# Performance work log

Measured on AMD Instinct MI355X. Metric: run time of the kernel, lower is better.

## Reference

```python
import jax, jax.numpy as jnp
import numpy as np

N, F, T, C = 20000, 4, 12, 256
HID, OUT = 128, 12
ER, E = 30000, 320000


def _gcn_agg(xw, src, dst, w):
    """GCNConv propagation with self-loops (weight 1): D^-1/2 (A+I) D^-1/2 @ xw.
    xw: [N, T, C] pre-projected features; src/dst: [E] int; w: [E] edge weights."""
    n = xw.shape[0]
    deg = jnp.zeros((n,), xw.dtype).at[dst].add(w) + 1.0  # +1 from self-loop
    dinv = jax.lax.rsqrt(deg)
    coef = (dinv[src] * w * dinv[dst])[:, None, None]      # [E,1,1]
    out = jnp.zeros_like(xw).at[dst].add(coef * xw[src])   # scatter-add messages
    return out + (dinv * dinv)[:, None, None] * xw         # self-loop term


def _regional_conv(x, Wc, bc, regs):
    # Shared GCNConv applied to each of the 5 state graphs, outputs summed.
    xw = jnp.einsum("nft,fc->ntc", x, Wc)  # [N, T, C], all periods at once
    out = bc
    for (src, dst, w) in regs:
        out = out + _gcn_agg(xw, src, dst, w)
    return out


def _forward(x, attrs, idxs, Wc_z, bc_z, Wl_z, bl_z, Wc_h, bc_h, Wl_h, bl_h,
             attention, W1, b1, W2, b2):
    regs = [(idx[0], idx[1], w) for idx, w in zip(idxs, attrs)]
    # A3TGCN runs an independent TGCN-GRU step per period from H=None (zeros),
    # then attention-averages over periods. With H=0:
    #   Z = sigmoid(linear_z([conv_z(X_t), 0]))   (hidden half of Wl drops out)
    #   reset gate R multiplies H=0, so it has no effect on the output
    #   H_tilde = tanh(linear_h([conv_h(X_t), 0]));  H_t = (1-Z)*H_tilde
    cz = _regional_conv(x, Wc_z, bc_z, regs)         # [N, T, C]
    Z = jax.nn.sigmoid(cz @ Wl_z[:C] + bl_z)
    ch = _regional_conv(x, Wc_h, bc_h, regs)
    Htilde = jnp.tanh(ch @ Wl_h[:C] + bl_h)
    Ht = (1.0 - Z) * Htilde                          # [N, T, C]
    probs = jax.nn.softmax(attention)                # [T]
    h = jnp.einsum("ntc,t->nc", Ht, probs)           # temporal attention pooling
    y = jax.nn.relu(h)
    y = jax.nn.relu(y @ W1 + b1)
    y = y @ W2 + b2
    return y, h


def setup_inputs():
    key = jax.random.key(0)
    ks = jax.random.split(key, 32)
    s = 0.05
    inp = {
        "x": jax.random.normal(ks[0], (N, F, T), jnp.float32),
        "edge_index": jax.random.randint(ks[1], (2, E), 0, N, jnp.int32),
    }
    regions = ["IA", "KS", "KY", "OH", "WI"]
    for i, nm in enumerate(regions):
        inp[nm + "edge_index"] = jax.random.randint(ks[2 + i], (2, ER), 0, N, jnp.int32)
    for i, nm in enumerate(regions):
        inp[nm + "edge_attr"] = jax.random.uniform(ks[7 + i], (ER,), jnp.float32)
    for gi, g in enumerate(["z", "r", "h"]):
        inp["Wc_" + g] = jax.random.normal(ks[12 + gi], (F, C), jnp.float32) * s
        inp["bc_" + g] = jnp.zeros((C,), jnp.float32)
        inp["Wl_" + g] = jax.random.normal(ks[15 + gi], (2 * C, C), jnp.float32) * s
        inp["bl_" + g] = jnp.zeros((C,), jnp.float32)
    inp["attention"] = jax.random.normal(ks[18], (T,), jnp.float32)
    inp["W1"] = jax.random.normal(ks[19], (C, HID), jnp.float32) * s
    inp["b1"] = jnp.zeros((HID,), jnp.float32)
    inp["W2"] = jax.random.normal(ks[20], (HID, OUT), jnp.float32) * s
    inp["b2"] = jnp.zeros((OUT,), jnp.float32)
    return inp


def reference(x, edge_index, IAedge_index, KSedge_index, KYedge_index, OHedge_index, WIedge_index,
              IAedge_attr, KSedge_attr, KYedge_attr, OHedge_attr, WIedge_attr,
              Wc_z, bc_z, Wl_z, bl_z, Wc_r, bc_r, Wl_r, bl_r, Wc_h, bc_h, Wl_h, bl_h,
              attention, W1, b1, W2, b2):
    # The full-graph edge_index and the reset-gate parameters are carried by the
    # original module but cannot influence the output (regional convs use the 5
    # state graphs; the reset gate multiplies the zero initial hidden state).
    idxs = [IAedge_index, KSedge_index, KYedge_index, OHedge_index, WIedge_index]
    attrs = [IAedge_attr, KSedge_attr, KYedge_attr, OHedge_attr, WIedge_attr]
    return _forward(x, attrs, idxs, Wc_z, bc_z, Wl_z, bl_z, Wc_h, bc_h, Wl_h, bl_h,
                    attention, W1, b1, W2, b2)
```

## Files before the change

### kernel.cpp

```cpp
#include <hip/hip_runtime.h>

constexpr int N    = 20000;
constexpr int T    = 12;
constexpr int C    = 256;
constexpr int HIDN = 128;
constexpr int OUTD = 12;
constexpr int ER   = 30000;
constexpr int NFT  = 48;
constexpr int EDGE_TOT = 5 * ER;
constexpr int CAP      = 32;
constexpr int EB       = 586;
constexpr int NT       = N / 16;

constexpr int WS_DEG    = 0;
constexpr int WS_CNT    = 100000;
constexpr int WS_MV     = 120000;
constexpr int WS_ZEND   = 122576;
constexpr int WS_WP     = 122576;
constexpr int WS_W2T    = 138960;
constexpr int WS_BUCKET = 140496;

constexpr float LOG2E = 1.4426950408889634f;

typedef __attribute__((ext_vector_type(8))) short short8;
typedef __attribute__((ext_vector_type(4))) float floatx4;
typedef __attribute__((ext_vector_type(2))) float floatx2;

#if __has_builtin(__builtin_amdgcn_exp2f)
#define EXP2(x) __builtin_amdgcn_exp2f(x)
#else
#define EXP2(x) exp2f(x)
#endif

__device__ __forceinline__ floatx2 pk_fma(floatx2 a, floatx2 b, floatx2 c) {
  floatx2 r;
  r.x = fmaf(a.x, b.x, c.x);
  r.y = fmaf(a.y, b.y, c.y);
  return r;
}

__device__ __forceinline__ short f2bf(float f) {
  unsigned u = __float_as_uint(f);
  u = u + 0x7fffu + ((u >> 16) & 1u);
  return (short)(u >> 16);
}

__device__ __forceinline__ void pick_region(
    int r,
    const int* e0, const int* e1, const int* e2, const int* e3, const int* e4,
    const float* a0, const float* a1, const float* a2, const float* a3, const float* a4,
    const int*& ei, const float*& ea) {
  switch (r) {
    case 0: ei = e0; ea = a0; break;
    case 1: ei = e1; ea = a1; break;
    case 2: ei = e2; ea = a2; break;
    case 3: ei = e3; ea = a3; break;
    default: ei = e4; ea = a4; break;
  }
}

__global__ void k_prep(
    const float* __restrict__ Wc_z, const float* __restrict__ bc_z,
    const float* __restrict__ Wl_z, const float* __restrict__ bl_z,
    const float* __restrict__ Wc_h, const float* __restrict__ bc_h,
    const float* __restrict__ Wl_h, const float* __restrict__ bl_h,
    const float* __restrict__ att, const float* __restrict__ W1,
    const float* __restrict__ W2,
    const int* __restrict__ e0, const int* __restrict__ e1,
    const int* __restrict__ e2, const int* __restrict__ e3,
    const int* __restrict__ e4,
    const float* __restrict__ a0, const float* __restrict__ a1,
    const float* __restrict__ a2, const float* __restrict__ a3,
    const float* __restrict__ a4,
    float* __restrict__ Mv, short* __restrict__ Wp, float* __restrict__ W2t,
    float* __restrict__ deg, int* __restrict__ cnt, int2* __restrict__ bucket) {
  int b = blockIdx.x, tid = threadIdx.x;
  if (b < 64) {
    int g  = b >> 5;
    int ch = b & 31;
    int k  = tid;
    const float* Wc = g ? Wc_h : Wc_z;
    const float* bc = g ? bc_h : bc_z;
    const float* Wl = g ? Wl_h : Wl_z;
    const float* bl = g ? bl_h : bl_z;
    float scale = g ? 2.0f * LOG2E : LOG2E;
    float m0 = 0.f, m1 = 0.f, m2 = 0.f, m3 = 0.f;
    float v = (ch == 0) ? bl[k] : 0.0f;
    int c0 = ch * 8;
#pragma unroll
    for (int cc = 0; cc < 8; cc++) {
      int c = c0 + cc;
      float wl = Wl[c * C + k];
      m0 = fmaf(Wc[0 * C + c], wl, m0);
      m1 = fmaf(Wc[1 * C + c], wl, m1);
      m2 = fmaf(Wc[2 * C + c], wl, m2);
      m3 = fmaf(Wc[3 * C + c], wl, m3);
      v  = fmaf(bc[c], wl, v);
    }
    float* o = Mv + g * (5 * C);
    atomicAdd(&o[0 * C + k], scale * m0);
    atomicAdd(&o[1 * C + k], scale * m1);
    atomicAdd(&o[2 * C + k], scale * m2);
    atomicAdd(&o[3 * C + k], scale * m3);
    atomicAdd(&o[4 * C + k], scale * v);
    return;
  }
  if (b == 64) {
    if (tid < T) {
      float amax = -3.0e38f;
      for (int t = 0; t < T; t++) amax = fmaxf(amax, att[t]);
      float s = 0.f;
      for (int t = 0; t < T; t++) s += __expf(att[t] - amax);
      Mv[10 * C + tid] = __expf(att[tid] - amax) / s;
    }
    return;
  }
  if (b < 200) {
    int idx = (b - 65) * 256 + tid;
    if (idx < 32768) {
      int j    = idx & 7;
      int lane = (idx >> 3) & 63;
      int ch   = (idx >> 9) & 7;
      int kt   = idx >> 12;
      int cin  = ch * 32 + (lane >> 4) * 8 + j;
      int kout = kt * 16 + (lane & 15);
      Wp[idx] = f2bf(W1[cin * HIDN + kout]);
    } else if (idx < 32768 + 1536) {
      int r = idx - 32768;
      int o = r >> 7, k = r & 127;
      W2t[r] = W2[k * OUTD + o];
    }
    return;
  }
  int i = (b - 200) * 256 + tid;
  if (i >= EDGE_TOT) return;
  int r = i / ER;
  int e = i - r * ER;
  const int* ei; const float* ea;
  pick_region(r, e0, e1, e2, e3, e4, a0, a1, a2, a3, a4, ei, ea);
  int src = ei[e];
  int dst = ei[ER + e];
  float w = ea[e];
  atomicAdd(&deg[r * N + dst], w);
  int slot = atomicAdd(&cnt[dst], 1);
  if (slot < CAP) bucket[dst * CAP + slot] = make_int2(src | (r << 15), __float_as_int(w));
}

__global__ __launch_bounds__(256) void k_fused(
    const float* __restrict__ x, const float* __restrict__ deg,
    const int* __restrict__ cnt, const int2* __restrict__ bucket,
    const float* __restrict__ Mv, const short* __restrict__ Wp,
    const float* __restrict__ b1, const float* __restrict__ W2t,
    const float* __restrict__ b2,
    float* __restrict__ y_out, float* __restrict__ h_out) {
  __shared__ float xs[16][NFT];
  __shared__ short hs[16][264];
  __shared__ float y1s[16][132];
  int tid = threadIdx.x;
  int wave = tid >> 6, lane = tid & 63;
  int n0 = blockIdx.x * 16;

  {
    int q = lane < NFT ? lane : NFT - 1;
    int sl = lane & (CAP - 1);
    int nb = n0 + wave * 4;
    int4 cv4 = *(const int4*)&cnt[nb];
    int cvs[4] = {cv4.x, cv4.y, cv4.z, cv4.w};
    int2 mrs[4];
#pragma unroll
    for (int nl = 0; nl < 4; nl++) mrs[nl] = bucket[(nb + nl) * CAP + sl];

#pragma unroll
    for (int nl = 0; nl < 4; nl++) {
      int rl = wave * 4 + nl;
      int n = nb + nl;
      float dd0 = rsqrtf(deg[0 * N + n] + 1.0f);
      float dd1 = rsqrtf(deg[1 * N + n] + 1.0f);
      float dd2 = rsqrtf(deg[2 * N + n] + 1.0f);
      float dd3 = rsqrtf(deg[3 * N + n] + 1.0f);
      float dd4 = rsqrtf(deg[4 * N + n] + 1.0f);
      float s = dd0 * dd0 + dd1 * dd1 + dd2 * dd2 + dd3 * dd3 + dd4 * dd4;
      float facc = s * x[n * NFT + q];

      int cv = cvs[nl];
      if (cv > CAP) cv = CAP;
      int2 m  = mrs[nl];
      bool valid = sl < cv;
      int key  = valid ? m.x : 0;
      int srcv = key & 0x7fff;
      int rr   = key >> 15;
      float dsrc = deg[rr * N + srcv];
      float ddn = rr == 0 ? dd0 : rr == 1 ? dd1 : rr == 2 ? dd2
                : rr == 3 ? dd3 : dd4;
      float cf = valid ? rsqrtf(dsrc + 1.0f) * __int_as_float(m.y) * ddn : 0.0f;

      float f1 = 0.f, f2 = 0.f, f3 = 0.f;
      int cvr = (cv + 3) & ~3;
      for (int j = 0; j < cvr; j += 4) {
        int s0 = __shfl(srcv, j);
        int s1 = __shfl(srcv, j + 1);
        int s2 = __shfl(srcv, j + 2);
        int s3 = __shfl(srcv, j + 3);
        float c0 = __shfl(cf, j);
        float c1 = __shfl(cf, j + 1);
        float c2 = __shfl(cf, j + 2);
        float c3 = __shfl(cf, j + 3);
        float x0 = x[s0 * NFT + q];
        float x1 = x[s1 * NFT + q];
        float x2 = x[s2 * NFT + q];
        float x3 = x[s3 * NFT + q];
        facc = fmaf(c0, x0, facc);
        f1 = fmaf(c1, x1, f1);
        f2 = fmaf(c2, x2, f2);
        f3 = fmaf(c3, x3, f3);
      }
      facc = (facc + f1) + (f2 + f3);
      if (lane < NFT) xs[rl][lane] = facc;
    }
  }
  __syncthreads();

  {
    int half = wave & 1;
    int nb   = (wave >> 1) * 8;
    int c0 = half * 128 + (lane << 1);
    const float* Mz = Mv;
    const float* Mh = Mv + 5 * C;
    floatx2 mz[4], mh[4], vz, vh;
#pragma unroll
    for (int f = 0; f < 4; f++) {
      mz[f] = *(const floatx2*)(Mz + f * C + c0);
      mh[f] = *(const floatx2*)(Mh + f * C + c0);
    }
    vz = *(const floatx2*)(Mz + 4 * C + c0);
    vh = *(const floatx2*)(Mh + 4 * C + c0);

#pragma unroll
    for (int nl = 0; nl < 8; nl++) {
      int rl = nb + nl;
      int n = n0 + rl;
      const float* xr = &xs[rl][0];
      floatx2 acc = {0.f, 0.f};
#pragma unroll
      for (int tb = 0; tb < 3; tb++) {
        float4 xf0 = *(const float4*)(xr + 0 * T + tb * 4);
        float4 xf1 = *(const float4*)(xr + 1 * T + tb * 4);
        float4 xf2 = *(const float4*)(xr + 2 * T + tb * 4);
        float4 xf3 = *(const float4*)(xr + 3 * T + tb * 4);
        float xs0[4] = {xf0.x, xf0.y, xf0.z, xf0.w};
        float xs1[4] = {xf1.x, xf1.y, xf1.z, xf1.w};
        float xs2[4] = {xf2.x, xf2.y, xf2.z, xf2.w};
        float xs3[4] = {xf3.x, xf3.y, xf3.z, xf3.w};
#pragma unroll
        for (int tt = 0; tt < 4; tt++) {
          int t = tb * 4 + tt;
          float p = Mv[10 * C + t];
          floatx2 x0 = {xs0[tt], xs0[tt]};
          floatx2 x1 = {xs1[tt], xs1[tt]};
          floatx2 x2 = {xs2[tt], xs2[tt]};
          floatx2 x3 = {xs3[tt], xs3[tt]};
          floatx2 az = pk_fma(mz[0], x0, pk_fma(mz[1], x1, pk_fma(mz[2], x2, pk_fma(mz[3], x3, vz))));
          floatx2 ah = pk_fma(mh[0], x0, pk_fma(mh[1], x1, pk_fma(mh[2], x2, pk_fma(mh[3], x3, vh))));
          floatx2 e1, e2;
          e1.x = EXP2(az.x); e1.y = EXP2(az.y);
          e2.x = EXP2(ah.x); e2.y = EXP2(ah.y);
          floatx2 one = {1.f, 1.f};
          floatx2 d1 = e1 + one;
          floatx2 d2 = e2 + one;
          floatx2 rD;
          rD.x = __builtin_amdgcn_rcpf(d1.x * d2.x);
          rD.y = __builtin_amdgcn_rcpf(d1.y * d2.y);
          floatx2 pv = {p, p};
          floatx2 pn = pk_fma(pv, e2, -pv);
          acc = pk_fma(pn, rD, acc);
        }
      }
      float2 o = {acc.x, acc.y};
      *(float2*)(h_out + n * C + c0) = o;
      unsigned pk = (unsigned short)f2bf(fmaxf(acc.x, 0.f)) |
                    ((unsigned)(unsigned short)f2bf(fmaxf(acc.y, 0.f)) << 16);
      *(unsigned*)&hs[rl][c0] = pk;
    }
  }
  __syncthreads();

  {
    int quad = lane >> 4, col = lane & 15;
    floatx4 acc2[2];
    acc2[0] = {0.f, 0.f, 0.f, 0.f};
    acc2[1] = {0.f, 0.f, 0.f, 0.f};
#pragma unroll
    for (int ch = 0; ch < 8; ch++) {
      short8 a = *(const short8*)&hs[col][ch * 32 + quad * 8];
#pragma unroll
      for (int kk = 0; kk < 2; kk++) {
        short8 bb = ((const short8*)Wp)[((wave * 2 + kk) * 8 + ch) * 64 + lane];
        acc2[kk] = __builtin_amdgcn_mfma_f32_16x16x32_bf16(a, bb, acc2[kk], 0, 0, 0);
      }
    }
#pragma unroll
    for (int kk = 0; kk < 2; kk++) {
      int kt = wave * 2 + kk;
      float bias = b1[kt * 16 + col];
#pragma unroll
      for (int r = 0; r < 4; r++)
        y1s[quad * 4 + r][kt * 16 + col] = fmaxf(acc2[kk][r] + bias, 0.f);
    }
  }
  __syncthreads();

  if (tid < 16 * OUTD) {
    int nl = tid / OUTD, o = tid - nl * OUTD;
    float sacc = b2[o];
    const float* yr = &y1s[nl][0];
    const float* wr = W2t + o * HIDN;
#pragma unroll 8
    for (int k4 = 0; k4 < 32; k4++) {
      float4 yv = *(const float4*)(yr + 4 * k4);
      float4 wv = *(const float4*)(wr + 4 * k4);
      sacc = fmaf(yv.x, wv.x, fmaf(yv.y, wv.y, fmaf(yv.z, wv.z, fmaf(yv.w, wv.w, sacc))));
    }
    y_out[(n0 + nl) * OUTD + o] = sacc;
  }
}

extern "C" void kernel_launch(void* const* d_in, const int* in_sizes, int n_in,
                              void* d_out, int out_size, void* d_ws, size_t ws_size,
                              hipStream_t stream) {
  const float* x   = (const float*)d_in[0];
  const int* eIA = (const int*)d_in[2];
  const int* eKS = (const int*)d_in[3];
  const int* eKY = (const int*)d_in[4];
  const int* eOH = (const int*)d_in[5];
  const int* eWI = (const int*)d_in[6];
  const float* aIA = (const float*)d_in[7];
  const float* aKS = (const float*)d_in[8];
  const float* aKY = (const float*)d_in[9];
  const float* aOH = (const float*)d_in[10];
  const float* aWI = (const float*)d_in[11];
  const float* Wc_z = (const float*)d_in[12];
  const float* bc_z = (const float*)d_in[13];
  const float* Wl_z = (const float*)d_in[14];
  const float* bl_z = (const float*)d_in[15];
  const float* Wc_h = (const float*)d_in[20];
  const float* bc_h = (const float*)d_in[21];
  const float* Wl_h = (const float*)d_in[22];
  const float* bl_h = (const float*)d_in[23];
  const float* att  = (const float*)d_in[24];
  const float* W1   = (const float*)d_in[25];
  const float* b1   = (const float*)d_in[26];
  const float* W2   = (const float*)d_in[27];
  const float* b2   = (const float*)d_in[28];

  float* ws     = (float*)d_ws;
  float* deg    = ws + WS_DEG;
  int*   cnt    = (int*)(ws + WS_CNT);
  float* Mv     = ws + WS_MV;
  short* Wp     = (short*)(ws + WS_WP);
  float* W2t    = ws + WS_W2T;
  int2*  bucket = (int2*)(ws + WS_BUCKET);

  float* y_out = (float*)d_out;
  float* h_out = y_out + N * OUTD;

  hipMemsetAsync(deg, 0, WS_ZEND * sizeof(float), stream);

  k_prep<<<200 + EB, 256, 0, stream>>>(Wc_z, bc_z, Wl_z, bl_z,
                                       Wc_h, bc_h, Wl_h, bl_h,
                                       att, W1, W2,
                                       eIA, eKS, eKY, eOH, eWI,
                                       aIA, aKS, aKY, aOH, aWI,
                                       Mv, Wp, W2t, deg, cnt, bucket);
  k_fused<<<NT, 256, 0, stream>>>(x, deg, cnt, bucket, Mv, Wp, b1, W2t, b2,
                                  y_out, h_out);
}
```

Before: 180.6 us.

## Restructure fused kernel to single-wave blocks of 4 nodes, dropping barriers

Changes k_fused from 256-thread blocks covering 16 nodes to 64-thread single-wave blocks covering 4 nodes, which removes all __syncthreads. The one wave now does the gather, then both channel halves of the gate computation, then all 8 MFMA column tiles of the first MLP layer. Only 4 of the 16 MFMA rows are used, so three quarters of the matrix work is padding, and Wp is reloaded by every block. The final dot product also gets four independent accumulators.

```diff
diff --git a/kernel.cpp b/kernel.cpp
--- a/kernel.cpp
+++ b/kernel.cpp
@@ -10,7 +10,7 @@
 constexpr int EDGE_TOT = 5 * ER;
 constexpr int CAP      = 32;
 constexpr int EB       = 586;
-constexpr int NT       = N / 16;
+constexpr int NB4      = N / 4;
 
 constexpr int WS_DEG    = 0;
 constexpr int WS_CNT    = 100000;
@@ -146,33 +146,30 @@
   if (slot < CAP) bucket[dst * CAP + slot] = make_int2(src | (r << 15), __float_as_int(w));
 }
 
-__global__ __launch_bounds__(256) void k_fused(
+__global__ __launch_bounds__(64) void k_fused(
     const float* __restrict__ x, const float* __restrict__ deg,
     const int* __restrict__ cnt, const int2* __restrict__ bucket,
     const float* __restrict__ Mv, const short* __restrict__ Wp,
     const float* __restrict__ b1, const float* __restrict__ W2t,
     const float* __restrict__ b2,
     float* __restrict__ y_out, float* __restrict__ h_out) {
-  __shared__ float xs[16][NFT];
-  __shared__ short hs[16][264];
-  __shared__ float y1s[16][132];
-  int tid = threadIdx.x;
-  int wave = tid >> 6, lane = tid & 63;
-  int n0 = blockIdx.x * 16;
+  __shared__ float xs[4][NFT];
+  __shared__ short hs[4][264];
+  __shared__ float y1s[4][132];
+  int lane = threadIdx.x;
+  int nb = blockIdx.x * 4;
 
   {
     int q = lane < NFT ? lane : NFT - 1;
     int sl = lane & (CAP - 1);
-    int nb = n0 + wave * 4;
     int4 cv4 = *(const int4*)&cnt[nb];
     int cvs[4] = {cv4.x, cv4.y, cv4.z, cv4.w};
     int2 mrs[4];
 #pragma unroll
     for (int nl = 0; nl < 4; nl++) mrs[nl] = bucket[(nb + nl) * CAP + sl];
 
-#pragma unroll
+#pragma unroll 1
     for (int nl = 0; nl < 4; nl++) {
-      int rl = wave * 4 + nl;
       int n = nb + nl;
       float dd0 = rsqrtf(deg[0 * N + n] + 1.0f);
       float dd1 = rsqrtf(deg[1 * N + n] + 1.0f);
@@ -215,15 +212,13 @@
         f3 = fmaf(c3, x3, f3);
       }
       facc = (facc + f1) + (f2 + f3);
-      if (lane < NFT) xs[rl][lane] = facc;
-    }
-  }
-  __syncthreads();
-
-  {
-    int half = wave & 1;
-    int nb   = (wave >> 1) * 8;
-    int c0 = half * 128 + (lane << 1);
+      if (lane < NFT) xs[nl][lane] = facc;
+    }
+  }
+
+#pragma unroll 1
+  for (int cp = 0; cp < 2; cp++) {
+    int c0 = cp * 128 + (lane << 1);
     const float* Mz = Mv;
     const float* Mh = Mv + 5 * C;
     floatx2 mz[4], mh[4], vz, vh;
@@ -236,10 +231,9 @@
     vh = *(const floatx2*)(Mh + 4 * C + c0);
 
 #pragma unroll
-    for (int nl = 0; nl < 8; nl++) {
-      int rl = nb + nl;
-      int n = n0 + rl;
-      const float* xr = &xs[rl][0];
+    for (int nl = 0; nl < 4; nl++) {
+      int n = nb + nl;
+      const float* xr = &xs[nl][0];
       floatx2 acc = {0.f, 0.f};
 #pragma unroll
       for (int tb = 0; tb < 3; tb++) {
@@ -279,48 +273,61 @@
       *(float2*)(h_out + n * C + c0) = o;
       unsigned pk = (unsigned short)f2bf(fmaxf(acc.x, 0.f)) |
                     ((unsigned)(unsigned short)f2bf(fmaxf(acc.y, 0.f)) << 16);
-      *(unsigned*)&hs[rl][c0] = pk;
-    }
-  }
-  __syncthreads();
+      *(unsigned*)&hs[nl][c0] = pk;
+    }
+  }
 
   {
     int quad = lane >> 4, col = lane & 15;
-    floatx4 acc2[2];
-    acc2[0] = {0.f, 0.f, 0.f, 0.f};
-    acc2[1] = {0.f, 0.f, 0.f, 0.f};
-#pragma unroll
-    for (int ch = 0; ch < 8; ch++) {
-      short8 a = *(const short8*)&hs[col][ch * 32 + quad * 8];
-#pragma unroll
-      for (int kk = 0; kk < 2; kk++) {
-        short8 bb = ((const short8*)Wp)[((wave * 2 + kk) * 8 + ch) * 64 + lane];
-        acc2[kk] = __builtin_amdgcn_mfma_f32_16x16x32_bf16(a, bb, acc2[kk], 0, 0, 0);
+    short8 z8 = {0, 0, 0, 0, 0, 0, 0, 0};
+#pragma unroll
+    for (int ktp = 0; ktp < 4; ktp++) {
+      floatx4 acc2[2];
+      acc2[0] = {0.f, 0.f, 0.f, 0.f};
+      acc2[1] = {0.f, 0.f, 0.f, 0.f};
+#pragma unroll
+      for (int ch = 0; ch < 8; ch++) {
+        short8 a = (col < 4) ? *(const short8*)&hs[col][ch * 32 + quad * 8] : z8;
+#pragma unroll
+        for (int kk = 0; kk < 2; kk++) {
+          short8 bb = ((const short8*)Wp)[((ktp * 2 + kk) * 8 + ch) * 64 + lane];
+          acc2[kk] = __builtin_amdgcn_mfma_f32_16x16x32_bf16(a, bb, acc2[kk], 0, 0, 0);
+        }
       }
-    }
-#pragma unroll
-    for (int kk = 0; kk < 2; kk++) {
-      int kt = wave * 2 + kk;
-      float bias = b1[kt * 16 + col];
-#pragma unroll
-      for (int r = 0; r < 4; r++)
-        y1s[quad * 4 + r][kt * 16 + col] = fmaxf(acc2[kk][r] + bias, 0.f);
-    }
-  }
-  __syncthreads();
-
-  if (tid < 16 * OUTD) {
-    int nl = tid / OUTD, o = tid - nl * OUTD;
-    float sacc = b2[o];
+      if (quad == 0) {
+#pragma unroll
+        for (int kk = 0; kk < 2; kk++) {
+          int kt = ktp * 2 + kk;
+          float bias = b1[kt * 16 + col];
+#pragma unroll
+          for (int r = 0; r < 4; r++)
+            y1s[r][kt * 16 + col] = fmaxf(acc2[kk][r] + bias, 0.f);
+        }
+      }
+    }
+  }
+
+  if (lane < 4 * OUTD) {
+    int nl = lane / OUTD, o = lane - nl * OUTD;
     const float* yr = &y1s[nl][0];
     const float* wr = W2t + o * HIDN;
-#pragma unroll 8
-    for (int k4 = 0; k4 < 32; k4++) {
-      float4 yv = *(const float4*)(yr + 4 * k4);
-      float4 wv = *(const float4*)(wr + 4 * k4);
-      sacc = fmaf(yv.x, wv.x, fmaf(yv.y, wv.y, fmaf(yv.z, wv.z, fmaf(yv.w, wv.w, sacc))));
-    }
-    y_out[(n0 + nl) * OUTD + o] = sacc;
+    float sa = b2[o], sb = 0.f, sc = 0.f, sd = 0.f;
+#pragma unroll
+    for (int k16 = 0; k16 < 128; k16 += 16) {
+      float4 y0 = *(const float4*)(yr + k16);
+      float4 w0 = *(const float4*)(wr + k16);
+      float4 y1 = *(const float4*)(yr + k16 + 4);
+      float4 w1 = *(const float4*)(wr + k16 + 4);
+      float4 y2 = *(const float4*)(yr + k16 + 8);
+      float4 w2 = *(const float4*)(wr + k16 + 8);
+      float4 y3 = *(const float4*)(yr + k16 + 12);
+      float4 w3 = *(const float4*)(wr + k16 + 12);
+      sa = fmaf(y0.x, w0.x, fmaf(y0.y, w0.y, fmaf(y0.z, w0.z, fmaf(y0.w, w0.w, sa))));
+      sb = fmaf(y1.x, w1.x, fmaf(y1.y, w1.y, fmaf(y1.z, w1.z, fmaf(y1.w, w1.w, sb))));
+      sc = fmaf(y2.x, w2.x, fmaf(y2.y, w2.y, fmaf(y2.z, w2.z, fmaf(y2.w, w2.w, sc))));
+      sd = fmaf(y3.x, w3.x, fmaf(y3.y, w3.y, fmaf(y3.z, w3.z, fmaf(y3.w, w3.w, sd))));
+    }
+    y_out[(nb + nl) * OUTD + o] = (sa + sb) + (sc + sd);
   }
 }
 
@@ -371,6 +378,6 @@
                                        eIA, eKS, eKY, eOH, eWI,
                                        aIA, aKS, aKY, aOH, aWI,
                                        Mv, Wp, W2t, deg, cnt, bucket);
-  k_fused<<<NT, 256, 0, stream>>>(x, deg, cnt, bucket, Mv, Wp, b1, W2t, b2,
+  k_fused<<<NB4, 64, 0, stream>>>(x, deg, cnt, bucket, Mv, Wp, b1, W2t, b2,
                                   y_out, h_out);
 }
```

Result: slower. 249.0 us (+37.9%).
